# Optimization experiments

Hardware: AMD Instinct MI355X
Metric: run time of the kernel (lower is better)

Reference implementation:

```python
import jax, jax.numpy as jnp
import numpy as np

N_NODES = 2048
DEG = 16
D = 4
E = N_NODES * DEG          # undirected edge count
TWO_E = 2 * E


def setup_inputs() -> dict:
    key = jax.random.key(0)
    # unique off-diagonal (row, col) pairs: sample from n*(n-1) index space
    rng = np.random.default_rng(0)
    p = rng.choice(N_NODES * (N_NODES - 1), size=E, replace=False)
    row = p // (N_NODES - 1)
    c = p % (N_NODES - 1)
    col = c + (c >= row)  # skip the diagonal -> no self loops, all pairs unique
    # edge_index: first E are (i->j), second E the reversed (j->i) in same order
    edge_index = jnp.asarray(
        np.stack([np.concatenate([row, col]), np.concatenate([col, row])]),
        dtype=jnp.int64 if jax.config.jax_enable_x64 else jnp.int32,
    )
    maps = jax.random.normal(key, (TWO_E, D, D), dtype=jnp.float32)
    return {"maps": maps, "edge_index": edge_index, "num_nodes": N_NODES}


def reference(maps, edge_index, num_nodes):
    n = num_nodes
    d = maps.shape[1]
    twoE = maps.shape[0]
    e = twoE // 2

    row_all = edge_index[0]
    # R^T R per directed edge  [2E, d, d]
    diag_contrib = jnp.einsum('eki,ekj->eij', maps, maps)
    # scatter-accumulate into per-node diagonal blocks  [n, d, d]
    maps_diag = jax.ops.segment_sum(diag_contrib, row_all, num_segments=n)

    row = edge_index[0, :e]
    col = edge_index[1, :e]
    # R_ij^T R_ji per undirected edge  [E, d, d]
    maps_triu = jnp.einsum('eki,ekj->eij', maps[:e], maps[e:])

    # eval-mode augmentation: identity
    to_inv = maps_diag + jnp.eye(d, dtype=maps.dtype)
    evals, evecs = jnp.linalg.eigh(to_inv)
    inv_root = jnp.clip(evals, 1e-8, None) ** -0.5
    # V diag(l^-1/2) V^T  [n, d, d]
    inv_sqrt = jnp.einsum('nik,nk,njk->nij', evecs, inv_root, evecs)

    maps_triu = inv_sqrt[row] @ maps_triu @ inv_sqrt[col]
    maps_diag = inv_sqrt @ maps_diag @ inv_sqrt
    maps_triu = jnp.clip(maps_triu, -1.0, 1.0)
    maps_diag = jnp.clip(maps_diag, -1.0, 1.0)

    # dense block Laplacian  [n, n, d, d] -> [n*d, n*d]
    L = jnp.zeros((n, n, d, d), dtype=maps.dtype)
    idx = jnp.arange(n)
    L = L.at[idx, idx].set(maps_diag)
    L = L.at[row, col].set(-maps_triu)
    L = L.at[col, row].set(-jnp.swapaxes(maps_triu, 1, 2))
    return L.transpose(0, 2, 1, 3).reshape(n * d, n * d)
```

## Files before the change

### kernel.cpp

```cpp
#include <hip/hip_runtime.h>
#include <math.h>


#define NNODES 2048
#define MAXDEG 96
#define BLK 256

typedef float vfloat4 __attribute__((ext_vector_type(4)));

__global__ void build_lists_kernel(const int* __restrict__ ei,
                                   int* __restrict__ lists,
                                   int* __restrict__ cnts,
                                   int E, int twoE) {
    int e = blockIdx.x * blockDim.x + threadIdx.x;
    if (e >= twoE) return;
    int node = ei[e];
    int nbr = ei[twoE + e];
    int t = (e >= E) ? 1 : 0;
    int u = t ? (e - E) : e;
    int slot = atomicAdd(&cnts[node], 1);
    if (slot < MAXDEG)
        lists[(size_t)node * MAXDEG + slot] = (nbr << 20) | (t << 19) | u;
}

template <int P, int Q>
__device__ __forceinline__ void jrot(float a[4][4], float v[4][4]) {
    float apq = a[P][Q];
    if (fabsf(apq) < 1e-12f) return;
    float theta = (a[Q][Q] - a[P][P]) / (2.0f * apq);
    float t = 1.0f / (fabsf(theta) + sqrtf(theta * theta + 1.0f));
    t = (theta < 0.0f) ? -t : t;
    float c = 1.0f / sqrtf(t * t + 1.0f);
    float s = t * c;
    #pragma unroll
    for (int k = 0; k < 4; ++k) {
        float akp = a[k][P], akq = a[k][Q];
        a[k][P] = c * akp - s * akq;
        a[k][Q] = s * akp + c * akq;
    }
    #pragma unroll
    for (int k = 0; k < 4; ++k) {
        float apk = a[P][k], aqk = a[Q][k];
        a[P][k] = c * apk - s * aqk;
        a[Q][k] = s * apk + c * aqk;
    }
    #pragma unroll
    for (int k = 0; k < 4; ++k) {
        float vkp = v[k][P], vkq = v[k][Q];
        v[k][P] = c * vkp - s * vkq;
        v[k][Q] = s * vkp + c * vkq;
    }
}

__global__ void __launch_bounds__(64)
node_kernel(const float* __restrict__ maps,
            const int* __restrict__ lists,
            const int* __restrict__ cnts,
            float* __restrict__ Smat,
            float* __restrict__ vdiag,
            int E, int n) {
    int node = blockIdx.x * blockDim.x + threadIdx.x;
    if (node >= n) return;
    float gm[4][4];
    #pragma unroll
    for (int i = 0; i < 4; ++i)
        #pragma unroll
        for (int j = 0; j < 4; ++j) gm[i][j] = 0.0f;
    int cnt = cnts[node];
    if (cnt > MAXDEG) cnt = MAXDEG;
    const int* myl = lists + (size_t)node * MAXDEG;
    #pragma unroll 4
    for (int j = 0; j < cnt; ++j) {
        int entry = myl[j];
        int t = (entry >> 19) & 1;
        int u = entry & 0x7FFF;
        int e = t ? (E + u) : u;
        const float4* mp = reinterpret_cast<const float4*>(maps + (size_t)e * 16);
        float4 q0 = mp[0], q1 = mp[1], q2 = mp[2], q3 = mp[3];
        float m[4][4] = {{q0.x, q0.y, q0.z, q0.w}, {q1.x, q1.y, q1.z, q1.w},
                         {q2.x, q2.y, q2.z, q2.w}, {q3.x, q3.y, q3.z, q3.w}};
        #pragma unroll
        for (int i = 0; i < 4; ++i)
            #pragma unroll
            for (int jj = 0; jj < 4; ++jj)
                gm[i][jj] += m[0][i] * m[0][jj] + m[1][i] * m[1][jj] +
                             m[2][i] * m[2][jj] + m[3][i] * m[3][jj];
    }
    float a[4][4], v[4][4];
    #pragma unroll
    for (int i = 0; i < 4; ++i)
        #pragma unroll
        for (int j = 0; j < 4; ++j) {
            a[i][j] = gm[i][j] + (i == j ? 1.0f : 0.0f);
            v[i][j] = (i == j) ? 1.0f : 0.0f;
        }
    #pragma unroll
    for (int sweep = 0; sweep < 6; ++sweep) {
        jrot<0, 1>(a, v); jrot<0, 2>(a, v); jrot<0, 3>(a, v);
        jrot<1, 2>(a, v); jrot<1, 3>(a, v); jrot<2, 3>(a, v);
    }
    float ir[4];
    #pragma unroll
    for (int m = 0; m < 4; ++m)
        ir[m] = 1.0f / sqrtf(fmaxf(a[m][m], 1e-8f));
    float s[4][4];
    #pragma unroll
    for (int i = 0; i < 4; ++i)
        #pragma unroll
        for (int j = 0; j < 4; ++j)
            s[i][j] = v[i][0] * v[j][0] * ir[0] + v[i][1] * v[j][1] * ir[1] +
                      v[i][2] * v[j][2] * ir[2] + v[i][3] * v[j][3] * ir[3];
    float4* sp = reinterpret_cast<float4*>(Smat + (size_t)node * 16);
    sp[0] = make_float4(s[0][0], s[0][1], s[0][2], s[0][3]);
    sp[1] = make_float4(s[1][0], s[1][1], s[1][2], s[1][3]);
    sp[2] = make_float4(s[2][0], s[2][1], s[2][2], s[2][3]);
    sp[3] = make_float4(s[3][0], s[3][1], s[3][2], s[3][3]);
    float t1[4][4];
    #pragma unroll
    for (int i = 0; i < 4; ++i)
        #pragma unroll
        for (int j = 0; j < 4; ++j)
            t1[i][j] = s[i][0] * gm[0][j] + s[i][1] * gm[1][j] +
                       s[i][2] * gm[2][j] + s[i][3] * gm[3][j];
    float4* vp = reinterpret_cast<float4*>(vdiag + (size_t)node * 16);
    #pragma unroll
    for (int i = 0; i < 4; ++i) {
        float r0 = t1[i][0] * s[0][0] + t1[i][1] * s[1][0] + t1[i][2] * s[2][0] + t1[i][3] * s[3][0];
        float r1 = t1[i][0] * s[0][1] + t1[i][1] * s[1][1] + t1[i][2] * s[2][1] + t1[i][3] * s[3][1];
        float r2 = t1[i][0] * s[0][2] + t1[i][1] * s[1][2] + t1[i][2] * s[2][2] + t1[i][3] * s[3][2];
        float r3 = t1[i][0] * s[0][3] + t1[i][1] * s[1][3] + t1[i][2] * s[2][3] + t1[i][3] * s[3][3];
        vp[i] = make_float4(fminf(fmaxf(r0, -1.0f), 1.0f),
                            fminf(fmaxf(r1, -1.0f), 1.0f),
                            fminf(fmaxf(r2, -1.0f), 1.0f),
                            fminf(fmaxf(r3, -1.0f), 1.0f));
    }
}

__global__ void __launch_bounds__(BLK)
writer_kernel(const float* __restrict__ maps,
              const int* __restrict__ lists,
              const int* __restrict__ cnts,
              const float* __restrict__ Smat,
              const float* __restrict__ vdiag,
              float* __restrict__ out, int E, int ld) {
    int r = blockIdx.x;
    int tid = threadIdx.x;
    __shared__ short colmap[NNODES];
    __shared__ vfloat4 s_dat[MAXDEG + 1][4];
    for (int i = tid; i < NNODES; i += BLK) colmap[i] = -1;

    int cnt = cnts[r];
    if (cnt > MAXDEG) cnt = MAXDEG;
    int col = -1, t = 0;
    if (tid < cnt) {
        int entry = lists[(size_t)r * MAXDEG + tid];
        col = entry >> 20;
        t = (entry >> 19) & 1;
        int u = entry & 0x7FFF;
        const float4* ap = reinterpret_cast<const float4*>(maps + (size_t)u * 16);
        const float4* bp = reinterpret_cast<const float4*>(maps + (size_t)(E + u) * 16);
        float4 a0 = ap[0], a1 = ap[1], a2 = ap[2], a3 = ap[3];
        float4 b0 = bp[0], b1 = bp[1], b2 = bp[2], b3 = bp[3];
        float A[4][4] = {{a0.x, a0.y, a0.z, a0.w}, {a1.x, a1.y, a1.z, a1.w},
                         {a2.x, a2.y, a2.z, a2.w}, {a3.x, a3.y, a3.z, a3.w}};
        float B[4][4] = {{b0.x, b0.y, b0.z, b0.w}, {b1.x, b1.y, b1.z, b1.w},
                         {b2.x, b2.y, b2.z, b2.w}, {b3.x, b3.y, b3.z, b3.w}};
        float C[4][4];
        #pragma unroll
        for (int i = 0; i < 4; ++i)
            #pragma unroll
            for (int j = 0; j < 4; ++j)
                C[i][j] = A[0][i] * B[0][j] + A[1][i] * B[1][j] +
                          A[2][i] * B[2][j] + A[3][i] * B[3][j];
        int rn = t ? col : r;
        int cn = t ? r : col;
        const float4* srp = reinterpret_cast<const float4*>(Smat + (size_t)rn * 16);
        const float4* scp = reinterpret_cast<const float4*>(Smat + (size_t)cn * 16);
        float4 s0 = srp[0], s1 = srp[1], s2 = srp[2], s3 = srp[3];
        float Sr[4][4] = {{s0.x, s0.y, s0.z, s0.w}, {s1.x, s1.y, s1.z, s1.w},
                          {s2.x, s2.y, s2.z, s2.w}, {s3.x, s3.y, s3.z, s3.w}};
        float4 c0 = scp[0], c1 = scp[1], c2 = scp[2], c3 = scp[3];
        float Sc[4][4] = {{c0.x, c0.y, c0.z, c0.w}, {c1.x, c1.y, c1.z, c1.w},
                          {c2.x, c2.y, c2.z, c2.w}, {c3.x, c3.y, c3.z, c3.w}};
        float t1m[4][4];
        #pragma unroll
        for (int i = 0; i < 4; ++i)
            #pragma unroll
            for (int j = 0; j < 4; ++j)
                t1m[i][j] = Sr[i][0] * C[0][j] + Sr[i][1] * C[1][j] +
                            Sr[i][2] * C[2][j] + Sr[i][3] * C[3][j];
        float W[4][4];
        #pragma unroll
        for (int i = 0; i < 4; ++i)
            #pragma unroll
            for (int j = 0; j < 4; ++j) {
                float x = t1m[i][0] * Sc[0][j] + t1m[i][1] * Sc[1][j] +
                          t1m[i][2] * Sc[2][j] + t1m[i][3] * Sc[3][j];
                W[i][j] = -fminf(fmaxf(x, -1.0f), 1.0f);
            }
        if (t) {
            s_dat[tid][0] = (vfloat4){W[0][0], W[1][0], W[2][0], W[3][0]};
            s_dat[tid][1] = (vfloat4){W[0][1], W[1][1], W[2][1], W[3][1]};
            s_dat[tid][2] = (vfloat4){W[0][2], W[1][2], W[2][2], W[3][2]};
            s_dat[tid][3] = (vfloat4){W[0][3], W[1][3], W[2][3], W[3][3]};
        } else {
            s_dat[tid][0] = (vfloat4){W[0][0], W[0][1], W[0][2], W[0][3]};
            s_dat[tid][1] = (vfloat4){W[1][0], W[1][1], W[1][2], W[1][3]};
            s_dat[tid][2] = (vfloat4){W[2][0], W[2][1], W[2][2], W[2][3]};
            s_dat[tid][3] = (vfloat4){W[3][0], W[3][1], W[3][2], W[3][3]};
        }
    }
    if (tid < 4) {
        float4 dv = reinterpret_cast<const float4*>(vdiag + (size_t)r * 16)[tid];
        s_dat[MAXDEG][tid] = (vfloat4){dv.x, dv.y, dv.z, dv.w};
    }
    __syncthreads();
    if (tid < cnt && !t) colmap[col] = (short)tid;
    __syncthreads();
    if (tid < cnt && t) colmap[col] = (short)tid;
    if (tid == 0) colmap[r] = MAXDEG;
    __syncthreads();

    size_t base = (size_t)(r * 4) * (size_t)ld;
    vfloat4* orow0 = reinterpret_cast<vfloat4*>(out + base);
    vfloat4* orow1 = reinterpret_cast<vfloat4*>(out + base + (size_t)ld);
    vfloat4* orow2 = reinterpret_cast<vfloat4*>(out + base + (size_t)2 * ld);
    vfloat4* orow3 = reinterpret_cast<vfloat4*>(out + base + (size_t)3 * ld);
    const vfloat4 zero = (vfloat4){0.f, 0.f, 0.f, 0.f};
    for (int cb = tid; cb < NNODES; cb += BLK) {
        int sl = colmap[cb];
        vfloat4 v0 = zero, v1 = zero, v2 = zero, v3 = zero;
        if (sl >= 0) {
            v0 = s_dat[sl][0]; v1 = s_dat[sl][1];
            v2 = s_dat[sl][2]; v3 = s_dat[sl][3];
        }
        __builtin_nontemporal_store(v0, &orow0[cb]);
        __builtin_nontemporal_store(v1, &orow1[cb]);
        __builtin_nontemporal_store(v2, &orow2[cb]);
        __builtin_nontemporal_store(v3, &orow3[cb]);
    }
}

extern "C" void kernel_launch(void* const* d_in, const int* in_sizes, int n_in,
                              void* d_out, int out_size, void* d_ws, size_t ws_size,
                              hipStream_t stream) {
    const float* maps = (const float*)d_in[0];
    const int* ei = (const int*)d_in[1];
    int twoE = in_sizes[0] / 16;
    int E = twoE / 2;
    int n = NNODES;
    int ld = n * 4;
    float* out = (float*)d_out;

    int*   ws_cnt  = (int*)d_ws;
    int*   ws_list = ws_cnt + n;
    float* ws_S    = (float*)(ws_list + (size_t)n * MAXDEG);
    float* ws_vd   = ws_S + (size_t)n * 16;

    (void)hipMemsetAsync(ws_cnt, 0, (size_t)n * sizeof(int), stream);
    build_lists_kernel<<<(twoE + BLK - 1) / BLK, BLK, 0, stream>>>(
        ei, ws_list, ws_cnt, E, twoE);
    node_kernel<<<(n + 63) / 64, 64, 0, stream>>>(
        maps, ws_list, ws_cnt, ws_S, ws_vd, E, n);
    writer_kernel<<<n, BLK, 0, stream>>>(
        maps, ws_list, ws_cnt, ws_S, ws_vd, out, E, ld);
}
```

Before: 102.5 us.

## Split per-edge block compute into separate edge kernel, simplify writer

```diff
diff --git a/kernel.cpp b/kernel.cpp
--- a/kernel.cpp
+++ b/kernel.cpp
@@ -137,10 +137,74 @@
 }
 
 __global__ void __launch_bounds__(BLK)
-writer_kernel(const float* __restrict__ maps,
-              const int* __restrict__ lists,
+edge_kernel(const float* __restrict__ maps,
+            const int* __restrict__ ei,
+            const float* __restrict__ Smat,
+            float* __restrict__ wdat,
+            int E, int twoE) {
+    int e = blockIdx.x * blockDim.x + threadIdx.x;
+    if (e >= twoE) return;
+    int t = (e >= E) ? 1 : 0;
+    int u = t ? (e - E) : e;
+    int rn = ei[u];
+    int cn = ei[twoE + u];
+    const float4* ap = reinterpret_cast<const float4*>(maps + (size_t)u * 16);
+    const float4* bp = reinterpret_cast<const float4*>(maps + (size_t)(E + u) * 16);
+    float4 a0 = ap[0], a1 = ap[1], a2 = ap[2], a3 = ap[3];
+    float4 b0 = bp[0], b1 = bp[1], b2 = bp[2], b3 = bp[3];
+    float A[4][4] = {{a0.x, a0.y, a0.z, a0.w}, {a1.x, a1.y, a1.z, a1.w},
+                     {a2.x, a2.y, a2.z, a2.w}, {a3.x, a3.y, a3.z, a3.w}};
+    float B[4][4] = {{b0.x, b0.y, b0.z, b0.w}, {b1.x, b1.y, b1.z, b1.w},
+                     {b2.x, b2.y, b2.z, b2.w}, {b3.x, b3.y, b3.z, b3.w}};
+    float C[4][4];
+    #pragma unroll
+    for (int i = 0; i < 4; ++i)
+        #pragma unroll
+        for (int j = 0; j < 4; ++j)
+            C[i][j] = A[0][i] * B[0][j] + A[1][i] * B[1][j] +
+                      A[2][i] * B[2][j] + A[3][i] * B[3][j];
+    const float4* srp = reinterpret_cast<const float4*>(Smat + (size_t)rn * 16);
+    const float4* scp = reinterpret_cast<const float4*>(Smat + (size_t)cn * 16);
+    float4 s0 = srp[0], s1 = srp[1], s2 = srp[2], s3 = srp[3];
+    float Sr[4][4] = {{s0.x, s0.y, s0.z, s0.w}, {s1.x, s1.y, s1.z, s1.w},
+                      {s2.x, s2.y, s2.z, s2.w}, {s3.x, s3.y, s3.z, s3.w}};
+    float4 c0 = scp[0], c1 = scp[1], c2 = scp[2], c3 = scp[3];
+    float Sc[4][4] = {{c0.x, c0.y, c0.z, c0.w}, {c1.x, c1.y, c1.z, c1.w},
+                      {c2.x, c2.y, c2.z, c2.w}, {c3.x, c3.y, c3.z, c3.w}};
+    float t1m[4][4];
+    #pragma unroll
+    for (int i = 0; i < 4; ++i)
+        #pragma unroll
+        for (int j = 0; j < 4; ++j)
+            t1m[i][j] = Sr[i][0] * C[0][j] + Sr[i][1] * C[1][j] +
+                        Sr[i][2] * C[2][j] + Sr[i][3] * C[3][j];
+    float W[4][4];
+    #pragma unroll
+    for (int i = 0; i < 4; ++i)
+        #pragma unroll
+        for (int j = 0; j < 4; ++j) {
+            float x = t1m[i][0] * Sc[0][j] + t1m[i][1] * Sc[1][j] +
+                      t1m[i][2] * Sc[2][j] + t1m[i][3] * Sc[3][j];
+            W[i][j] = -fminf(fmaxf(x, -1.0f), 1.0f);
+        }
+    float4* wp = reinterpret_cast<float4*>(wdat + (size_t)e * 16);
+    if (t) {
+        wp[0] = make_float4(W[0][0], W[1][0], W[2][0], W[3][0]);
+        wp[1] = make_float4(W[0][1], W[1][1], W[2][1], W[3][1]);
+        wp[2] = make_float4(W[0][2], W[1][2], W[2][2], W[3][2]);
+        wp[3] = make_float4(W[0][3], W[1][3], W[2][3], W[3][3]);
+    } else {
+        wp[0] = make_float4(W[0][0], W[0][1], W[0][2], W[0][3]);
+        wp[1] = make_float4(W[1][0], W[1][1], W[1][2], W[1][3]);
+        wp[2] = make_float4(W[2][0], W[2][1], W[2][2], W[2][3]);
+        wp[3] = make_float4(W[3][0], W[3][1], W[3][2], W[3][3]);
+    }
+}
+
+__global__ void __launch_bounds__(BLK, 8)
+writer_kernel(const int* __restrict__ lists,
               const int* __restrict__ cnts,
-              const float* __restrict__ Smat,
+              const float* __restrict__ wdat,
               const float* __restrict__ vdiag,
               float* __restrict__ out, int E, int ld) {
     int r = blockIdx.x;
@@ -157,58 +221,12 @@
         col = entry >> 20;
         t = (entry >> 19) & 1;
         int u = entry & 0x7FFF;
-        const float4* ap = reinterpret_cast<const float4*>(maps + (size_t)u * 16);
-        const float4* bp = reinterpret_cast<const float4*>(maps + (size_t)(E + u) * 16);
-        float4 a0 = ap[0], a1 = ap[1], a2 = ap[2], a3 = ap[3];
-        float4 b0 = bp[0], b1 = bp[1], b2 = bp[2], b3 = bp[3];
-        float A[4][4] = {{a0.x, a0.y, a0.z, a0.w}, {a1.x, a1.y, a1.z, a1.w},
-                         {a2.x, a2.y, a2.z, a2.w}, {a3.x, a3.y, a3.z, a3.w}};
-        float B[4][4] = {{b0.x, b0.y, b0.z, b0.w}, {b1.x, b1.y, b1.z, b1.w},
-                         {b2.x, b2.y, b2.z, b2.w}, {b3.x, b3.y, b3.z, b3.w}};
-        float C[4][4];
-        #pragma unroll
-        for (int i = 0; i < 4; ++i)
-            #pragma unroll
-            for (int j = 0; j < 4; ++j)
-                C[i][j] = A[0][i] * B[0][j] + A[1][i] * B[1][j] +
-                          A[2][i] * B[2][j] + A[3][i] * B[3][j];
-        int rn = t ? col : r;
-        int cn = t ? r : col;
-        const float4* srp = reinterpret_cast<const float4*>(Smat + (size_t)rn * 16);
-        const float4* scp = reinterpret_cast<const float4*>(Smat + (size_t)cn * 16);
-        float4 s0 = srp[0], s1 = srp[1], s2 = srp[2], s3 = srp[3];
-        float Sr[4][4] = {{s0.x, s0.y, s0.z, s0.w}, {s1.x, s1.y, s1.z, s1.w},
-                          {s2.x, s2.y, s2.z, s2.w}, {s3.x, s3.y, s3.z, s3.w}};
-        float4 c0 = scp[0], c1 = scp[1], c2 = scp[2], c3 = scp[3];
-        float Sc[4][4] = {{c0.x, c0.y, c0.z, c0.w}, {c1.x, c1.y, c1.z, c1.w},
-                          {c2.x, c2.y, c2.z, c2.w}, {c3.x, c3.y, c3.z, c3.w}};
-        float t1m[4][4];
-        #pragma unroll
-        for (int i = 0; i < 4; ++i)
-            #pragma unroll
-            for (int j = 0; j < 4; ++j)
-                t1m[i][j] = Sr[i][0] * C[0][j] + Sr[i][1] * C[1][j] +
-                            Sr[i][2] * C[2][j] + Sr[i][3] * C[3][j];
-        float W[4][4];
-        #pragma unroll
-        for (int i = 0; i < 4; ++i)
-            #pragma unroll
-            for (int j = 0; j < 4; ++j) {
-                float x = t1m[i][0] * Sc[0][j] + t1m[i][1] * Sc[1][j] +
-                          t1m[i][2] * Sc[2][j] + t1m[i][3] * Sc[3][j];
-                W[i][j] = -fminf(fmaxf(x, -1.0f), 1.0f);
-            }
-        if (t) {
-            s_dat[tid][0] = (vfloat4){W[0][0], W[1][0], W[2][0], W[3][0]};
-            s_dat[tid][1] = (vfloat4){W[0][1], W[1][1], W[2][1], W[3][1]};
-            s_dat[tid][2] = (vfloat4){W[0][2], W[1][2], W[2][2], W[3][2]};
-            s_dat[tid][3] = (vfloat4){W[0][3], W[1][3], W[2][3], W[3][3]};
-        } else {
-            s_dat[tid][0] = (vfloat4){W[0][0], W[0][1], W[0][2], W[0][3]};
-            s_dat[tid][1] = (vfloat4){W[1][0], W[1][1], W[1][2], W[1][3]};
-            s_dat[tid][2] = (vfloat4){W[2][0], W[2][1], W[2][2], W[2][3]};
-            s_dat[tid][3] = (vfloat4){W[3][0], W[3][1], W[3][2], W[3][3]};
-        }
+        int e = t ? (E + u) : u;
+        const vfloat4* wp = reinterpret_cast<const vfloat4*>(wdat + (size_t)e * 16);
+        s_dat[tid][0] = wp[0];
+        s_dat[tid][1] = wp[1];
+        s_dat[tid][2] = wp[2];
+        s_dat[tid][3] = wp[3];
     }
     if (tid < 4) {
         float4 dv = reinterpret_cast<const float4*>(vdiag + (size_t)r * 16)[tid];
@@ -234,10 +252,10 @@
             v0 = s_dat[sl][0]; v1 = s_dat[sl][1];
             v2 = s_dat[sl][2]; v3 = s_dat[sl][3];
         }
-        __builtin_nontemporal_store(v0, &orow0[cb]);
-        __builtin_nontemporal_store(v1, &orow1[cb]);
-        __builtin_nontemporal_store(v2, &orow2[cb]);
-        __builtin_nontemporal_store(v3, &orow3[cb]);
+        orow0[cb] = v0;
+        orow1[cb] = v1;
+        orow2[cb] = v2;
+        orow3[cb] = v3;
     }
 }
 
@@ -256,12 +274,15 @@
     int*   ws_list = ws_cnt + n;
     float* ws_S    = (float*)(ws_list + (size_t)n * MAXDEG);
     float* ws_vd   = ws_S + (size_t)n * 16;
+    float* ws_wdat = ws_vd + (size_t)n * 16;
 
     (void)hipMemsetAsync(ws_cnt, 0, (size_t)n * sizeof(int), stream);
     build_lists_kernel<<<(twoE + BLK - 1) / BLK, BLK, 0, stream>>>(
         ei, ws_list, ws_cnt, E, twoE);
     node_kernel<<<(n + 63) / 64, 64, 0, stream>>>(
         maps, ws_list, ws_cnt, ws_S, ws_vd, E, n);
+    edge_kernel<<<(twoE + BLK - 1) / BLK, BLK, 0, stream>>>(
+        maps, ei, ws_S, ws_wdat, E, twoE);
     writer_kernel<<<n, BLK, 0, stream>>>(
-        maps, ws_list, ws_cnt, ws_S, ws_vd, out, E, ld);
-}
+        ws_list, ws_cnt, ws_wdat, ws_vd, out, E, ld);
+}
```

Result: no change. 101.1 us (-1.4%).
